# Kernel optimization log

Hardware: AMD Instinct MI355X
Metric: run time of the kernel (lower is better)

Reference implementation:

```python
import jax, jax.numpy as jnp
import numpy as np

BN_EPS = 1e-5


def setup_inputs() -> dict:
    key = jax.random.key(0)
    ks = jax.random.split(key, 9)
    C = 256
    x = jax.random.normal(ks[0], (4, C, 56, 56), jnp.float32)
    Wq = jax.random.normal(ks[1], (C // 4, C), jnp.float32) * 0.05
    Wk = jax.random.normal(ks[2], (C // 4, C), jnp.float32) * 0.05
    Wv = jax.random.normal(ks[3], (C, 2 * C), jnp.float32) * 0.05
    bv = jax.random.normal(ks[4], (C,), jnp.float32) * 0.05
    gamma = jnp.ones((C,), jnp.float32)
    beta = jnp.zeros((C,), jnp.float32)
    rmean = jax.random.normal(ks[5], (C,), jnp.float32) * 0.05
    rvar = jax.random.uniform(ks[6], (C,), jnp.float32) + 0.5
    return {"x": x, "Wq": Wq, "Wk": Wk, "Wv": Wv, "bv": bv,
            "gamma": gamma, "beta": beta, "rmean": rmean, "rvar": rvar, "k": 7}


def _patches(t, k):
    # t: [b, c, h, w] -> [b, c, k*k, h, w], zero-padded neighborhoods (matches F.unfold row-major order)
    b, c, h, w = t.shape
    p = (k - 1) // 2
    tp = jnp.pad(t, ((0, 0), (0, 0), (p, p), (p, p)))
    return jnp.stack([tp[:, :, i:i + h, j:j + w] for i in range(k) for j in range(k)], axis=2)


def _align(ta, tb, k, Wq, Wk):
    b, c, h, w = ta.shape
    hw = h * w
    # query token per pixel: [b, hw, 1, c]
    spta = ta.reshape(b, c, hw).transpose(0, 2, 1)[:, :, None, :]
    # unfolded k^2 neighborhood of tb: [b, hw, k2, c]
    pt = _patches(tb, k).reshape(b, c, k * k, hw).transpose(0, 3, 2, 1)
    keys = jnp.concatenate([spta, pt], axis=2)          # [b, hw, 1+k2, c]
    q = jnp.einsum('bnqc,dc->bnqd', spta, Wq)           # [b, hw, 1, c/4]
    kk = jnp.einsum('bnkc,dc->bnkd', keys, Wk)          # [b, hw, 1+k2, c/4]
    attn = jax.nn.softmax(jnp.einsum('bnqd,bnkd->bnqk', q, kk), axis=-1)
    out = jnp.einsum('bnqk,bnkc->bnqc', attn[..., 1:], pt)  # drop self-key column
    return out[:, :, 0, :].transpose(0, 2, 1).reshape(b, c, h, w)


def reference(x, Wq, Wk, Wv, bv, gamma, beta, rmean, rvar, k):
    xt1, xt2 = jnp.split(x, 2, axis=0)
    xt1 = _align(xt2, xt1, k, Wq, Wk)   # note: second call uses the freshly aligned xt1 (as in source)
    xt2 = _align(xt1, xt2, k, Wq, Wk)
    xt = jnp.concatenate([xt1, xt2], axis=0)
    cat = jnp.concatenate([x, xt], axis=1)              # [2B, 2C, H, W]
    y = jnp.einsum('bchw,oc->bohw', cat, Wv) + bv[None, :, None, None]
    scale = (gamma / jnp.sqrt(rvar + BN_EPS))[None, :, None, None]
    y = (y - rmean[None, :, None, None]) * scale + beta[None, :, None, None]
    return jax.nn.relu(y)
```

## Files before the change

### kernel.cpp

```cpp
#include <hip/hip_runtime.h>
#include <hip/hip_bf16.h>

#define HW 3136
#define W56 56

typedef __attribute__((ext_vector_type(8))) short short8;
typedef __attribute__((ext_vector_type(4))) float f32x4;

static __device__ __forceinline__ f32x4 mfma16(short8 a, short8 b, f32x4 c) {
    return __builtin_amdgcn_mfma_f32_16x16x32_bf16(a, b, c, 0, 0, 0);
}
static __device__ __forceinline__ float b2f(unsigned short u) {
    unsigned int x = ((unsigned int)u) << 16;
    return __builtin_bit_cast(float, x);
}
static __device__ __forceinline__ unsigned short f2b(float f) {
    __hip_bfloat16 h = __float2bfloat16(f);
    return *(unsigned short*)&h;
}

__global__ __launch_bounds__(256) void prep(const float* __restrict__ x,
                                            const float* __restrict__ Wq, const float* __restrict__ Wk,
                                            const float* __restrict__ Wv,
                                            unsigned short* __restrict__ catb,
                                            unsigned short* __restrict__ xlo,
                                            unsigned short* __restrict__ Wqk_hi,
                                            unsigned short* __restrict__ Wqk_lo,
                                            unsigned short* __restrict__ Wvb) {
    __shared__ float tile[32][33];
    int bx = blockIdx.x, tid = threadIdx.x;
    if (bx < 3136) {
        int b = bx / 784, rem = bx % 784;
        int p0 = (rem >> 3) * 32, c0 = (rem & 7) * 32;
        int tx = tid & 31, ty = tid >> 5;
#pragma unroll
        for (int i = ty; i < 32; i += 8)
            tile[i][tx] = x[((size_t)b * 256 + c0 + i) * HW + p0 + tx];
        __syncthreads();
        int pxl = tid >> 3, cg = tid & 7;
        ushort4 h4, l4;
#pragma unroll
        for (int u = 0; u < 4; ++u) {
            float v = tile[cg * 4 + u][pxl];
            unsigned short hi = f2b(v);
            ((unsigned short*)&h4)[u] = hi;
            ((unsigned short*)&l4)[u] = f2b(v - b2f(hi));
        }
        size_t row = (size_t)b * HW + p0 + pxl;
        *(ushort4*)&catb[row * 512 + c0 + cg * 4] = h4;
        *(ushort4*)&xlo[row * 256 + c0 + cg * 4] = l4;
    } else {
        int i = (bx - 3136) * 256 + tid;
        if (i < 32768) {
            float w = (i < 16384) ? Wq[i] : Wk[i - 16384];
            unsigned short hi = f2b(w);
            Wqk_hi[i] = hi;
            Wqk_lo[i] = f2b(w - b2f(hi));
        }
        if (i < 131072) Wvb[i] = f2b(Wv[i]);
    }
}

__global__ __launch_bounds__(256) void projqk(const unsigned short* __restrict__ Whi,
                                              const unsigned short* __restrict__ Wlo,
                                              const unsigned short* __restrict__ Bhi_g, int bstr,
                                              const unsigned short* __restrict__ Blo_g,
                                              float* __restrict__ Qout,
                                              unsigned short* __restrict__ Kout) {
    __shared__ short Ahi[64][72], Alo[64][72];
    __shared__ short Bhi[32][72], Blo[32][72];
    int tid = threadIdx.x, lane = tid & 63, wv = tid >> 6;
    int l15 = lane & 15, lk = (lane >> 4) * 8;
    int pxb = blockIdx.x * 32;
    int y64 = blockIdx.y * 64;
    int ar0 = tid >> 3, ac = (tid & 7) * 8;
    int br = tid >> 3, bc = (tid & 7) * 8;
    f32x4 acc[2];
    acc[0] = (f32x4){0.f, 0.f, 0.f, 0.f};
    acc[1] = (f32x4){0.f, 0.f, 0.f, 0.f};

    short8 rAh0 = *(const short8*)(Whi + (size_t)(y64 + ar0) * 256 + ac);
    short8 rAl0 = *(const short8*)(Wlo + (size_t)(y64 + ar0) * 256 + ac);
    short8 rAh1 = *(const short8*)(Whi + (size_t)(y64 + ar0 + 32) * 256 + ac);
    short8 rAl1 = *(const short8*)(Wlo + (size_t)(y64 + ar0 + 32) * 256 + ac);
    short8 rBh  = *(const short8*)(Bhi_g + (size_t)(pxb + br) * bstr + bc);
    short8 rBl  = *(const short8*)(Blo_g + (size_t)(pxb + br) * 256 + bc);

#pragma unroll
    for (int t = 0; t < 4; ++t) {
        *(short8*)&Ahi[ar0][ac] = rAh0;      *(short8*)&Alo[ar0][ac] = rAl0;
        *(short8*)&Ahi[ar0 + 32][ac] = rAh1; *(short8*)&Alo[ar0 + 32][ac] = rAl1;
        *(short8*)&Bhi[br][bc] = rBh;        *(short8*)&Blo[br][bc] = rBl;
        __syncthreads();
        if (t < 3) {
            int kn = t * 64 + 64;
            rAh0 = *(const short8*)(Whi + (size_t)(y64 + ar0) * 256 + kn + ac);
            rAl0 = *(const short8*)(Wlo + (size_t)(y64 + ar0) * 256 + kn + ac);
            rAh1 = *(const short8*)(Whi + (size_t)(y64 + ar0 + 32) * 256 + kn + ac);
            rAl1 = *(const short8*)(Wlo + (size_t)(y64 + ar0 + 32) * 256 + kn + ac);
            rBh  = *(const short8*)(Bhi_g + (size_t)(pxb + br) * bstr + kn + bc);
            rBl  = *(const short8*)(Blo_g + (size_t)(pxb + br) * 256 + kn + bc);
        }
#pragma unroll
        for (int ks = 0; ks < 2; ++ks) {
            short8 ah = *(const short8*)&Ahi[wv * 16 + l15][ks * 32 + lk];
            short8 al = *(const short8*)&Alo[wv * 16 + l15][ks * 32 + lk];
            short8 bh[2], bl[2];
#pragma unroll
            for (int j = 0; j < 2; ++j) {
                bh[j] = *(const short8*)&Bhi[j * 16 + l15][ks * 32 + lk];
                bl[j] = *(const short8*)&Blo[j * 16 + l15][ks * 32 + lk];
            }
#pragma unroll
            for (int j = 0; j < 2; ++j) {
                acc[j] = mfma16(ah, bh[j], acc[j]);
                acc[j] = mfma16(ah, bl[j], acc[j]);
                acc[j] = mfma16(al, bh[j], acc[j]);
            }
        }
        __syncthreads();
    }
    int d0 = wv * 16 + (lane >> 4) * 4;
    if (blockIdx.y == 0) {
#pragma unroll
        for (int j = 0; j < 2; ++j) {
            int px = pxb + j * 16 + l15;
            *(f32x4*)(Qout + (size_t)px * 64 + d0) = acc[j];
        }
    } else {
#pragma unroll
        for (int j = 0; j < 2; ++j) {
            int px = pxb + j * 16 + l15;
            ushort4 kb;
            kb.x = f2b(acc[j][0]); kb.y = f2b(acc[j][1]);
            kb.z = f2b(acc[j][2]); kb.w = f2b(acc[j][3]);
            *(ushort4*)(Kout + (size_t)px * 64 + d0) = kb;
        }
    }
}

__global__ __launch_bounds__(256) void attn_kernel(const float* __restrict__ Q,
                                                   const unsigned short* __restrict__ Kb,
                                                   int selfOff, int kbOff,
                                                   const unsigned short* __restrict__ V,
                                                   unsigned short* __restrict__ outb,
                                                   unsigned short* __restrict__ outlo) {
    __shared__ float wsh[4][64];
    __shared__ int njsh[4][64];
    int tid = threadIdx.x, lane = tid & 63, wv = tid >> 6;
    int nbc = gridDim.x >> 3;
    int lb = (blockIdx.x & 7) * nbc + (blockIdx.x >> 3);
    int gw = lb * 4 + wv;
    int b = gw / HW, pix = gw % HW;
    int py = pix / W56, px = pix % W56;

    int valid = 0, nj = 0;
    if (lane == 0) {
        valid = 1;
    } else if (lane < 50) {
        int d = lane - 1, dy = d / 7 - 3, dx = d % 7 - 3;
        int ny = py + dy, nx = px + dx;
        if (ny >= 0 && ny < W56 && nx >= 0 && nx < W56) { valid = 1; nj = ny * W56 + nx; }
    }
    njsh[wv][lane] = nj;

    int rg = lane >> 3, c8 = lane & 7;
    f32x4 qf0 = *(const f32x4*)(Q + (size_t)gw * 64 + c8 * 8);
    f32x4 qf1 = *(const f32x4*)(Q + (size_t)gw * 64 + c8 * 8 + 4);
    short8 kvv[7];
#pragma unroll
    for (int i = 0; i < 7; ++i) {
        int j = i * 8 + rg;
        int row = (i == 0 && rg == 0) ? (selfOff + gw) : (kbOff + b * HW + njsh[wv][j]);
        kvv[i] = *(const short8*)(Kb + (size_t)row * 64 + c8 * 8);
    }

    __builtin_amdgcn_s_setprio(1);

    float pl[7];
#pragma unroll
    for (int i = 0; i < 7; ++i) {
        float pA = b2f((unsigned short)kvv[i][0]) * qf0[0] + b2f((unsigned short)kvv[i][1]) * qf0[1] +
                   b2f((unsigned short)kvv[i][2]) * qf0[2] + b2f((unsigned short)kvv[i][3]) * qf0[3];
        float pB = b2f((unsigned short)kvv[i][4]) * qf1[0] + b2f((unsigned short)kvv[i][5]) * qf1[1] +
                   b2f((unsigned short)kvv[i][6]) * qf1[2] + b2f((unsigned short)kvv[i][7]) * qf1[3];
        pl[i] = pA + pB;
    }
#pragma unroll
    for (int off = 1; off < 8; off <<= 1)
#pragma unroll
        for (int i = 0; i < 7; ++i) pl[i] += __shfl_xor(pl[i], off);
    float myl = 0.f;
#pragma unroll
    for (int i = 0; i < 7; ++i) myl = (c8 == i) ? pl[i] : myl;
    float tl = __shfl(myl, ((lane & 7) << 3) | (lane >> 3));

    float logit = (lane < 50 && valid) ? tl : 0.f;
    float m = (lane < 50) ? logit : -1e30f;
#pragma unroll
    for (int off = 32; off; off >>= 1) m = fmaxf(m, __shfl_xor(m, off));
    float e = (lane < 50) ? __expf(logit - m) : 0.f;
    float s = e;
#pragma unroll
    for (int off = 32; off; off >>= 1) s += __shfl_xor(s, off);
    float w = (lane >= 1 && lane < 50 && valid) ? e / s : 0.f;
    wsh[wv][lane] = w;

    int h = lane >> 5, l32 = lane & 31;
    int jb = h * 25;
    float av[8];
#pragma unroll
    for (int cc = 0; cc < 8; ++cc) av[cc] = 0.f;
    const unsigned short* vb = V + (size_t)b * HW * 512 + l32 * 8;
#pragma unroll
    for (int g = 0; g < 2; ++g) {
        float wj[12];
        short8 vj[12];
#pragma unroll
        for (int u = 0; u < 12; ++u) {
            int j = jb + g * 12 + u;
            wj[u] = wsh[wv][j];
            vj[u] = *(const short8*)(vb + (size_t)njsh[wv][j] * 512);
        }
#pragma unroll
        for (int u = 0; u < 12; ++u)
#pragma unroll
            for (int cc = 0; cc < 8; ++cc)
                av[cc] += wj[u] * b2f((unsigned short)vj[u][cc]);
    }
    {
        int j = jb + 24;
        float wt = wsh[wv][j];
        short8 vt = *(const short8*)(vb + (size_t)njsh[wv][j] * 512);
#pragma unroll
        for (int cc = 0; cc < 8; ++cc) av[cc] += wt * b2f((unsigned short)vt[cc]);
    }
#pragma unroll
    for (int cc = 0; cc < 8; ++cc) av[cc] += __shfl_xor(av[cc], 32);

    __builtin_amdgcn_s_setprio(0);

    if (h == 0) {
        short8 pk, lo8;
#pragma unroll
        for (int cc = 0; cc < 8; ++cc) {
            unsigned short hi = f2b(av[cc]);
            pk[cc] = (short)hi;
            lo8[cc] = (short)f2b(av[cc] - b2f(hi));
        }
        *(short8*)(outb + (size_t)gw * 512 + l32 * 8) = pk;
        if (outlo) *(short8*)(outlo + (size_t)gw * 256 + l32 * 8) = lo8;
    }
}

__global__ __launch_bounds__(256) void conv_mfma(const unsigned short* __restrict__ catb,
                                                 const unsigned short* __restrict__ Wvb,
                                                 const float* __restrict__ bv, const float* __restrict__ gamma,
                                                 const float* __restrict__ beta, const float* __restrict__ rmean,
                                                 const float* __restrict__ rvar, float* __restrict__ out) {
    __shared__ short Ald[64][72];
    __shared__ short Bld[64][72];
    int tid = threadIdx.x, lane = tid & 63, wv = tid >> 6;
    int wm = wv >> 1, wn = wv & 1;
    int l15 = lane & 15, lk = (lane >> 4) * 8;
    int n0g = blockIdx.x * 64;
    int m0g = blockIdx.y * 64;
    f32x4 acc[2][2];
#pragma unroll
    for (int i = 0; i < 2; ++i)
#pragma unroll
        for (int j = 0; j < 2; ++j) acc[i][j] = (f32x4){0.f, 0.f, 0.f, 0.f};

    float sc_[2][4], sh_[2][4];
#pragma unroll
    for (int i = 0; i < 2; ++i) {
        int ob = m0g + wm * 32 + i * 16 + (lane >> 4) * 4;
#pragma unroll
        for (int r = 0; r < 4; ++r) {
            int o = ob + r;
            float s = gamma[o] * rsqrtf(rvar[o] + 1e-5f);
            sc_[i][r] = s;
            sh_[i][r] = (bv[o] - rmean[o]) * s + beta[o];
        }
    }

    for (int kt = 0; kt < 512; kt += 64) {
#pragma unroll
        for (int s = 0; s < 2; ++s) {
            int q = tid + 256 * s;
            int r = q >> 3, c = (q & 7) * 8;
            *(short8*)&Ald[r][c] = *(const short8*)(Wvb + (size_t)(m0g + r) * 512 + kt + c);
            *(short8*)&Bld[r][c] = *(const short8*)(catb + (size_t)(n0g + r) * 512 + kt + c);
        }
        __syncthreads();
#pragma unroll
        for (int ks = 0; ks < 2; ++ks) {
            short8 a[2], b[2];
#pragma unroll
            for (int i = 0; i < 2; ++i) a[i] = *(const short8*)&Ald[wm * 32 + i * 16 + l15][ks * 32 + lk];
#pragma unroll
            for (int j = 0; j < 2; ++j) b[j] = *(const short8*)&Bld[wn * 32 + j * 16 + l15][ks * 32 + lk];
#pragma unroll
            for (int i = 0; i < 2; ++i)
#pragma unroll
                for (int j = 0; j < 2; ++j) acc[i][j] = mfma16(a[i], b[j], acc[i][j]);
        }
        __syncthreads();
    }
#pragma unroll
    for (int i = 0; i < 2; ++i) {
        int ob = m0g + wm * 32 + i * 16 + (lane >> 4) * 4;
#pragma unroll
        for (int j = 0; j < 2; ++j) {
            int px = n0g + wn * 32 + j * 16 + l15;
            int b = px / HW, p = px - b * HW;
            f32x4 v = acc[i][j];
#pragma unroll
            for (int r = 0; r < 4; ++r) {
                out[((size_t)(b * 256 + ob + r)) * HW + p] = fmaxf(v[r] * sc_[i][r] + sh_[i][r], 0.f);
            }
        }
    }
}

extern "C" void kernel_launch(void* const* d_in, const int* in_sizes, int n_in,
                              void* d_out, int out_size, void* d_ws, size_t ws_size,
                              hipStream_t stream) {
    const float* x     = (const float*)d_in[0];
    const float* Wq    = (const float*)d_in[1];
    const float* Wk    = (const float*)d_in[2];
    const float* Wv    = (const float*)d_in[3];
    const float* bv    = (const float*)d_in[4];
    const float* gamma = (const float*)d_in[5];
    const float* beta  = (const float*)d_in[6];
    const float* rmean = (const float*)d_in[7];
    const float* rvar  = (const float*)d_in[8];
    float* out = (float*)d_out;

    float* Qall = (float*)d_ws;
    float* Qn   = Qall + (size_t)4 * HW * 64;
    unsigned short* Kb = (unsigned short*)(Qn + (size_t)2 * HW * 64);
    unsigned short* catb   = Kb + (size_t)6 * HW * 64;
    unsigned short* xlo    = catb + (size_t)4 * HW * 512;
    unsigned short* xt1lo  = xlo + (size_t)4 * HW * 256;
    unsigned short* Wqk_hi = xt1lo + (size_t)2 * HW * 256;
    unsigned short* Wqk_lo = Wqk_hi + 128 * 256;
    unsigned short* Wvb    = Wqk_lo + 128 * 256;

    prep<<<3648, 256, 0, stream>>>(x, Wq, Wk, Wv, catb, xlo, Wqk_hi, Wqk_lo, Wvb);

    projqk<<<dim3(392, 2), 256, 0, stream>>>(Wqk_hi, Wqk_lo, catb, 512, xlo, Qall, Kb);

    attn_kernel<<<1568, 256, 0, stream>>>(Qall + (size_t)2 * HW * 64, Kb,
                                          2 * HW, 0,
                                          catb, catb + 256, xt1lo);

    projqk<<<dim3(196, 2), 256, 0, stream>>>(Wqk_hi, Wqk_lo, catb + 256, 512, xt1lo,
                                             Qn, Kb + (size_t)4 * HW * 64);

    attn_kernel<<<1568, 256, 0, stream>>>(Qn, Kb,
                                          4 * HW, 2 * HW,
                                          catb + (size_t)2 * HW * 512,
                                          catb + (size_t)2 * HW * 512 + 256, nullptr);

    conv_mfma<<<dim3(196, 4), 256, 0, stream>>>(catb, Wvb, bv, gamma, beta, rmean, rvar, out);
}
```

Before: 59.98 us.

## Fuse second attention pass with batch 0-1 conv blocks in one launch

Refactors the attention and conv kernels into device bodies, then launches one kernel whose first 1568 blocks run the second attention pass and whose remaining blocks compute the 1x1 conv for images 0-1, which depend only on data already finished. The conv for images 2-3 runs in a separate, smaller launch afterwards. This is meant to overlap independent conv work with the gather-bound attention and to fill the tail of that launch. The cost is a larger shared-memory footprint for the attention blocks, which could lower occupancy, plus one extra launch.

```diff
diff --git a/kernel.cpp b/kernel.cpp
--- a/kernel.cpp
+++ b/kernel.cpp
@@ -139,17 +139,16 @@
     }
 }
 
-__global__ __launch_bounds__(256) void attn_kernel(const float* __restrict__ Q,
-                                                   const unsigned short* __restrict__ Kb,
-                                                   int selfOff, int kbOff,
-                                                   const unsigned short* __restrict__ V,
-                                                   unsigned short* __restrict__ outb,
-                                                   unsigned short* __restrict__ outlo) {
-    __shared__ float wsh[4][64];
-    __shared__ int njsh[4][64];
-    int tid = threadIdx.x, lane = tid & 63, wv = tid >> 6;
-    int nbc = gridDim.x >> 3;
-    int lb = (blockIdx.x & 7) * nbc + (blockIdx.x >> 3);
+static __device__ __forceinline__ void attn_body(int lb, int tid, char* smem,
+                                                 const float* __restrict__ Q,
+                                                 const unsigned short* __restrict__ Kb,
+                                                 int selfOff, int kbOff,
+                                                 const unsigned short* __restrict__ V,
+                                                 unsigned short* __restrict__ outb,
+                                                 unsigned short* __restrict__ outlo) {
+    float* wsh = (float*)smem;
+    int* njsh = (int*)(smem + 1024);
+    int lane = tid & 63, wv = tid >> 6;
     int gw = lb * 4 + wv;
     int b = gw / HW, pix = gw % HW;
     int py = pix / W56, px = pix % W56;
@@ -162,7 +161,7 @@
         int ny = py + dy, nx = px + dx;
         if (ny >= 0 && ny < W56 && nx >= 0 && nx < W56) { valid = 1; nj = ny * W56 + nx; }
     }
-    njsh[wv][lane] = nj;
+    njsh[wv * 64 + lane] = nj;
 
     int rg = lane >> 3, c8 = lane & 7;
     f32x4 qf0 = *(const f32x4*)(Q + (size_t)gw * 64 + c8 * 8);
@@ -171,7 +170,7 @@
 #pragma unroll
     for (int i = 0; i < 7; ++i) {
         int j = i * 8 + rg;
-        int row = (i == 0 && rg == 0) ? (selfOff + gw) : (kbOff + b * HW + njsh[wv][j]);
+        int row = (i == 0 && rg == 0) ? (selfOff + gw) : (kbOff + b * HW + njsh[wv * 64 + j]);
         kvv[i] = *(const short8*)(Kb + (size_t)row * 64 + c8 * 8);
     }
 
@@ -204,7 +203,7 @@
 #pragma unroll
     for (int off = 32; off; off >>= 1) s += __shfl_xor(s, off);
     float w = (lane >= 1 && lane < 50 && valid) ? e / s : 0.f;
-    wsh[wv][lane] = w;
+    wsh[wv * 64 + lane] = w;
 
     int h = lane >> 5, l32 = lane & 31;
     int jb = h * 25;
@@ -219,8 +218,8 @@
 #pragma unroll
         for (int u = 0; u < 12; ++u) {
             int j = jb + g * 12 + u;
-            wj[u] = wsh[wv][j];
-            vj[u] = *(const short8*)(vb + (size_t)njsh[wv][j] * 512);
+            wj[u] = wsh[wv * 64 + j];
+            vj[u] = *(const short8*)(vb + (size_t)njsh[wv * 64 + j] * 512);
         }
 #pragma unroll
         for (int u = 0; u < 12; ++u)
@@ -230,8 +229,8 @@
     }
     {
         int j = jb + 24;
-        float wt = wsh[wv][j];
-        short8 vt = *(const short8*)(vb + (size_t)njsh[wv][j] * 512);
+        float wt = wsh[wv * 64 + j];
+        short8 vt = *(const short8*)(vb + (size_t)njsh[wv * 64 + j] * 512);
 #pragma unroll
         for (int cc = 0; cc < 8; ++cc) av[cc] += wt * b2f((unsigned short)vt[cc]);
     }
@@ -253,18 +252,17 @@
     }
 }
 
-__global__ __launch_bounds__(256) void conv_mfma(const unsigned short* __restrict__ catb,
+static __device__ __forceinline__ void conv_body(int n0g, int m0g, int tid, char* smem,
+                                                 const unsigned short* __restrict__ catb,
                                                  const unsigned short* __restrict__ Wvb,
                                                  const float* __restrict__ bv, const float* __restrict__ gamma,
                                                  const float* __restrict__ beta, const float* __restrict__ rmean,
                                                  const float* __restrict__ rvar, float* __restrict__ out) {
-    __shared__ short Ald[64][72];
-    __shared__ short Bld[64][72];
-    int tid = threadIdx.x, lane = tid & 63, wv = tid >> 6;
+    short(*Ald)[72] = (short(*)[72])smem;
+    short(*Bld)[72] = (short(*)[72])(smem + 64 * 72 * 2);
+    int lane = tid & 63, wv = tid >> 6;
     int wm = wv >> 1, wn = wv & 1;
     int l15 = lane & 15, lk = (lane >> 4) * 8;
-    int n0g = blockIdx.x * 64;
-    int m0g = blockIdx.y * 64;
     f32x4 acc[2][2];
 #pragma unroll
     for (int i = 0; i < 2; ++i)
@@ -321,6 +319,53 @@
             }
         }
     }
+}
+
+__global__ __launch_bounds__(256) void attn_kernel(const float* __restrict__ Q,
+                                                   const unsigned short* __restrict__ Kb,
+                                                   int selfOff, int kbOff,
+                                                   const unsigned short* __restrict__ V,
+                                                   unsigned short* __restrict__ outb,
+                                                   unsigned short* __restrict__ outlo) {
+    __shared__ __align__(16) char smem[2048];
+    int bx = blockIdx.x;
+    int lb = (bx & 7) * 196 + (bx >> 3);
+    attn_body(lb, threadIdx.x, smem, Q, Kb, selfOff, kbOff, V, outb, outlo);
+}
+
+__global__ __launch_bounds__(256) void attn2_conv01(const float* __restrict__ Q,
+                                                    const unsigned short* __restrict__ Kb,
+                                                    int selfOff, int kbOff,
+                                                    const unsigned short* __restrict__ V,
+                                                    unsigned short* __restrict__ outb,
+                                                    const unsigned short* __restrict__ catb,
+                                                    const unsigned short* __restrict__ Wvb,
+                                                    const float* __restrict__ bv, const float* __restrict__ gamma,
+                                                    const float* __restrict__ beta, const float* __restrict__ rmean,
+                                                    const float* __restrict__ rvar, float* __restrict__ out) {
+    __shared__ __align__(16) char smem[2 * 64 * 72 * 2];
+    int bx = blockIdx.x;
+    if (bx < 1568) {
+        int lb = (bx & 7) * 196 + (bx >> 3);
+        attn_body(lb, threadIdx.x, smem, Q, Kb, selfOff, kbOff, V, outb, nullptr);
+    } else {
+        int cb = bx - 1568;
+        int n0g = (cb >> 2) * 64;
+        int m0g = (cb & 3) * 64;
+        conv_body(n0g, m0g, threadIdx.x, smem, catb, Wvb, bv, gamma, beta, rmean, rvar, out);
+    }
+}
+
+__global__ __launch_bounds__(256) void conv_mfma(const unsigned short* __restrict__ catb,
+                                                 const unsigned short* __restrict__ Wvb,
+                                                 const float* __restrict__ bv, const float* __restrict__ gamma,
+                                                 const float* __restrict__ beta, const float* __restrict__ rmean,
+                                                 const float* __restrict__ rvar, float* __restrict__ out,
+                                                 int n_base) {
+    __shared__ __align__(16) char smem[2 * 64 * 72 * 2];
+    int n0g = n_base + blockIdx.x * 64;
+    int m0g = blockIdx.y * 64;
+    conv_body(n0g, m0g, threadIdx.x, smem, catb, Wvb, bv, gamma, beta, rmean, rvar, out);
 }
 
 extern "C" void kernel_launch(void* const* d_in, const int* in_sizes, int n_in,
@@ -358,10 +403,12 @@
     projqk<<<dim3(196, 2), 256, 0, stream>>>(Wqk_hi, Wqk_lo, catb + 256, 512, xt1lo,
                                              Qn, Kb + (size_t)4 * HW * 64);
 
-    attn_kernel<<<1568, 256, 0, stream>>>(Qn, Kb,
-                                          4 * HW, 2 * HW,
-                                          catb + (size_t)2 * HW * 512,
-                                          catb + (size_t)2 * HW * 512 + 256, nullptr);
-
-    conv_mfma<<<dim3(196, 4), 256, 0, stream>>>(catb, Wvb, bv, gamma, beta, rmean, rvar, out);
-}
+    attn2_conv01<<<1960, 256, 0, stream>>>(Qn, Kb,
+                                           4 * HW, 2 * HW,
+                                           catb + (size_t)2 * HW * 512,
+                                           catb + (size_t)2 * HW * 512 + 256,
+                                           catb, Wvb, bv, gamma, beta, rmean, rvar, out);
+
+    conv_mfma<<<dim3(98, 4), 256, 0, stream>>>(catb, Wvb, bv, gamma, beta, rmean, rvar, out,
+                                               98 * 64);
+}
```

Result: slower. 65.48 us (+9.2%).
